# Performance work log

Hardware: AMD Instinct MI355X
Metric: run time of the kernel (lower is better)

The kernel has to match this reference:

```python
import jax, jax.numpy as jnp
import numpy as np

SIGMA_SPATIAL = 1.0
SIGMA_BILATERAL = 0.25
RADIUS = 1
PATCH = 2 * RADIUS + 1  # 3


def _spatial_kernel():
    x, y = np.mgrid[-RADIUS:RADIUS + 1, -RADIUS:RADIUS + 1]
    w1 = np.exp(-(x ** 2 + y ** 2) / (2.0 * SIGMA_SPATIAL ** 2))
    return jnp.asarray(w1.reshape(-1), dtype=jnp.float32)  # [PATCH*PATCH]


def _extract_patches(x):
    # x: [B,H,W,C] -> [B,H,W,PATCH*PATCH,C] via reflect-padded shifted slices
    B, H, W, C = x.shape
    xp = jnp.pad(x, ((0, 0), (RADIUS, RADIUS), (RADIUS, RADIUS), (0, 0)), mode='reflect')
    return jnp.stack(
        [xp[:, dy:dy + H, dx:dx + W, :] for dy in range(PATCH) for dx in range(PATCH)],
        axis=3,
    )


def setup_inputs() -> dict:
    key = jax.random.key(0)
    k1, k2 = jax.random.split(key)
    src = jax.random.uniform(k1, (2, 512, 512, 21), dtype=jnp.float32)
    im = jax.random.uniform(k2, (2, 512, 512, 3), dtype=jnp.float32)
    return {"src": src, "im": im}


def reference(src, im):
    w1 = _spatial_kernel()  # [9]
    im_patches = _extract_patches(im)                      # [B,H,W,9,Ci]
    diff2 = jnp.sum((im_patches - im[:, :, :, None, :]) ** 2, axis=-1)  # [B,H,W,9]
    w = jnp.exp(-diff2 / (2.0 * SIGMA_BILATERAL ** 2)) * w1            # [B,H,W,9]
    src_patches = _extract_patches(src)                    # [B,H,W,9,Cs]
    num = jnp.sum(src_patches * w[..., None], axis=3)      # [B,H,W,Cs]
    den = jnp.sum(w, axis=3, keepdims=True)                # [B,H,W,1]
    return num / den
```

## Files before the change

kernel.cpp:

```cpp
#include <hip/hip_runtime.h>

#define BATCH 2
#define H 512
#define W 512
#define CS 21
#define CI 3
#define P 256
#define TPB 256
#define NCH 6

__device__ __forceinline__ int reflect1(int v, int n) {
    if (v < 0) v = -v;
    else if (v >= n) v = 2 * n - 2 - v;
    return v;
}

__device__ __forceinline__ void fma4(float4& a, const float4 v, const float w) {
    a.x = fmaf(v.x, w, a.x);
    a.y = fmaf(v.y, w, a.y);
    a.z = fmaf(v.z, w, a.z);
    a.w = fmaf(v.w, w, a.w);
}

__global__ __launch_bounds__(TPB) void jbu_kernel(
    const float* __restrict__ src, const float* __restrict__ im,
    float* __restrict__ out)
{
    __shared__ __align__(16) float s_im[3][P + 2][CI];
    __shared__ __align__(16) float s_w[P][12];

    const int t  = threadIdx.x;
    const int x0 = blockIdx.x * P;
    const int y  = blockIdx.y;
    const int b  = blockIdx.z;

    const int ry0 = reflect1(y - 1, H);
    const int ry2 = reflect1(y + 1, H);

    for (int i = t; i < 3 * (P + 2) * CI; i += TPB) {
        int r   = i / ((P + 2) * CI);
        int rem = i - r * ((P + 2) * CI);
        int col = rem / CI;
        int ch  = rem - col * CI;
        int ry  = (r == 0) ? ry0 : ((r == 1) ? y : ry2);
        int gx  = reflect1(x0 + col - 1, W);
        s_im[r][col][ch] = im[((b * H + ry) * W + gx) * CI + ch];
    }
    __syncthreads();

    {
        const float w1k[9] = {0.36787944f, 0.60653066f, 0.36787944f,
                              0.60653066f, 1.0f,        0.60653066f,
                              0.36787944f, 0.60653066f, 0.36787944f};
        const float c0 = s_im[1][t + 1][0];
        const float c1 = s_im[1][t + 1][1];
        const float c2 = s_im[1][t + 1][2];
        float wv[9];
        float den = 0.f;
        #pragma unroll
        for (int k = 0; k < 9; ++k) {
            const int dy = k / 3, dx = k % 3;
            float d0 = s_im[dy][t + dx][0] - c0;
            float d1 = s_im[dy][t + dx][1] - c1;
            float d2 = s_im[dy][t + dx][2] - c2;
            float w = __expf(-8.0f * (d0 * d0 + d1 * d1 + d2 * d2)) * w1k[k];
            wv[k] = w;
            den += w;
        }
        const float inv = 1.0f / den;
        float4 wa = {wv[0] * inv, wv[1] * inv, wv[2] * inv, wv[3] * inv};
        float4 wb = {wv[4] * inv, wv[5] * inv, wv[6] * inv, wv[7] * inv};
        *(float4*)&s_w[t][0] = wa;
        *(float4*)&s_w[t][4] = wb;
        s_w[t][8] = wv[8] * inv;
    }
    __syncthreads();

    const float* row0 = src + (size_t)(b * H + ry0) * (W * CS);
    const float* row1 = src + (size_t)(b * H + y  ) * (W * CS);
    const float* row2 = src + (size_t)(b * H + ry2) * (W * CS);
    float*       orow = out + (size_t)(b * H + y  ) * (W * CS);

    for (int wi = t; wi < P * NCH; wi += TPB) {
        int p = wi / NCH;
        int q = wi - p * NCH;
        int coff = (q == 5) ? 17 : (q << 2);
        int x  = x0 + p;
        int xm = (x == 0)     ? 1     : x - 1;
        int xp = (x == W - 1) ? W - 2 : x + 1;
        int om = xm * CS + coff;
        int oc = x  * CS + coff;
        int op = xp * CS + coff;

        const float4 wA = *(const float4*)&s_w[p][0];
        const float4 wB = *(const float4*)&s_w[p][4];
        const float  w8 = s_w[p][8];

        float4 v0 = *(const float4*)(row0 + om);
        float4 v1 = *(const float4*)(row0 + oc);
        float4 v2 = *(const float4*)(row0 + op);
        float4 v3 = *(const float4*)(row1 + om);
        float4 v4 = *(const float4*)(row1 + oc);
        float4 v5 = *(const float4*)(row1 + op);
        float4 v6 = *(const float4*)(row2 + om);
        float4 v7 = *(const float4*)(row2 + oc);
        float4 v8 = *(const float4*)(row2 + op);

        float4 acc = {0.f, 0.f, 0.f, 0.f};
        fma4(acc, v0, wA.x);
        fma4(acc, v1, wA.y);
        fma4(acc, v2, wA.z);
        fma4(acc, v3, wA.w);
        fma4(acc, v4, wB.x);
        fma4(acc, v5, wB.y);
        fma4(acc, v6, wB.z);
        fma4(acc, v7, wB.w);
        fma4(acc, v8, w8);

        *(float4*)(orow + oc) = acc;
    }
}

extern "C" void kernel_launch(void* const* d_in, const int* in_sizes, int n_in,
                              void* d_out, int out_size, void* d_ws, size_t ws_size,
                              hipStream_t stream) {
    const float* src = (const float*)d_in[0];
    const float* im  = (const float*)d_in[1];
    float* out = (float*)d_out;
    dim3 grid(W / P, H, BATCH);
    jbu_kernel<<<grid, TPB, 0, stream>>>(src, im, out);
}
```

Measured before the change: 114.7 us.

## Remap blocks so each XCD handles contiguous rows and alias shared buffers

```diff
diff --git a/kernel.cpp b/kernel.cpp
--- a/kernel.cpp
+++ b/kernel.cpp
@@ -9,12 +9,6 @@
 #define TPB 256
 #define NCH 6
 
-__device__ __forceinline__ int reflect1(int v, int n) {
-    if (v < 0) v = -v;
-    else if (v >= n) v = 2 * n - 2 - v;
-    return v;
-}
-
 __device__ __forceinline__ void fma4(float4& a, const float4 v, const float w) {
     a.x = fmaf(v.x, w, a.x);
     a.y = fmaf(v.y, w, a.y);
@@ -22,58 +16,71 @@
     a.w = fmaf(v.w, w, a.w);
 }
 
-__global__ __launch_bounds__(TPB) void jbu_kernel(
+__global__ __launch_bounds__(TPB, 8) void jbu_kernel(
     const float* __restrict__ src, const float* __restrict__ im,
     float* __restrict__ out)
 {
-    __shared__ __align__(16) float s_im[3][P + 2][CI];
-    __shared__ __align__(16) float s_w[P][12];
+    __shared__ __align__(16) float s_buf[P * 12];
 
-    const int t  = threadIdx.x;
-    const int x0 = blockIdx.x * P;
-    const int y  = blockIdx.y;
-    const int b  = blockIdx.z;
+    const int t = threadIdx.x;
 
-    const int ry0 = reflect1(y - 1, H);
-    const int ry2 = reflect1(y + 1, H);
+    const int f   = blockIdx.x;
+    const int xcd = f & 7;
+    const int g   = f >> 3;
+    const int y   = (xcd << 6) | (g & 63);
+    const int r   = g >> 6;
+    const int x0  = (r & 1) * P;
+    const int b   = r >> 1;
 
+    const int ry0 = (y == 0)     ? 1     : y - 1;
+    const int ry2 = (y == H - 1) ? H - 2 : y + 1;
+
+    const float* imb = im + (size_t)b * H * W * CI;
     for (int i = t; i < 3 * (P + 2) * CI; i += TPB) {
-        int r   = i / ((P + 2) * CI);
-        int rem = i - r * ((P + 2) * CI);
+        int row = i / ((P + 2) * CI);
+        int rem = i - row * ((P + 2) * CI);
         int col = rem / CI;
         int ch  = rem - col * CI;
-        int ry  = (r == 0) ? ry0 : ((r == 1) ? y : ry2);
-        int gx  = reflect1(x0 + col - 1, W);
-        s_im[r][col][ch] = im[((b * H + ry) * W + gx) * CI + ch];
+        int ry  = (row == 0) ? ry0 : ((row == 1) ? y : ry2);
+        int gx  = x0 + col - 1;
+        gx = (gx < 0) ? 1 : ((gx >= W) ? W - 2 : gx);
+        s_buf[i] = imb[(ry * W + gx) * CI + ch];
     }
     __syncthreads();
 
+    float4 wa, wb;
+    float w8n;
     {
         const float w1k[9] = {0.36787944f, 0.60653066f, 0.36787944f,
                               0.60653066f, 1.0f,        0.60653066f,
                               0.36787944f, 0.60653066f, 0.36787944f};
-        const float c0 = s_im[1][t + 1][0];
-        const float c1 = s_im[1][t + 1][1];
-        const float c2 = s_im[1][t + 1][2];
+        const int cbase = ((P + 2) + t + 1) * CI;
+        const float c0 = s_buf[cbase + 0];
+        const float c1 = s_buf[cbase + 1];
+        const float c2 = s_buf[cbase + 2];
         float wv[9];
         float den = 0.f;
         #pragma unroll
         for (int k = 0; k < 9; ++k) {
             const int dy = k / 3, dx = k % 3;
-            float d0 = s_im[dy][t + dx][0] - c0;
-            float d1 = s_im[dy][t + dx][1] - c1;
-            float d2 = s_im[dy][t + dx][2] - c2;
+            const int idx = (dy * (P + 2) + t + dx) * CI;
+            float d0 = s_buf[idx + 0] - c0;
+            float d1 = s_buf[idx + 1] - c1;
+            float d2 = s_buf[idx + 2] - c2;
             float w = __expf(-8.0f * (d0 * d0 + d1 * d1 + d2 * d2)) * w1k[k];
             wv[k] = w;
             den += w;
         }
         const float inv = 1.0f / den;
-        float4 wa = {wv[0] * inv, wv[1] * inv, wv[2] * inv, wv[3] * inv};
-        float4 wb = {wv[4] * inv, wv[5] * inv, wv[6] * inv, wv[7] * inv};
-        *(float4*)&s_w[t][0] = wa;
-        *(float4*)&s_w[t][4] = wb;
-        s_w[t][8] = wv[8] * inv;
+        wa = make_float4(wv[0] * inv, wv[1] * inv, wv[2] * inv, wv[3] * inv);
+        wb = make_float4(wv[4] * inv, wv[5] * inv, wv[6] * inv, wv[7] * inv);
+        w8n = wv[8] * inv;
     }
+    __syncthreads();
+
+    *(float4*)&s_buf[t * 12 + 0] = wa;
+    *(float4*)&s_buf[t * 12 + 4] = wb;
+    s_buf[t * 12 + 8] = w8n;
     __syncthreads();
 
     const float* row0 = src + (size_t)(b * H + ry0) * (W * CS);
@@ -92,9 +99,9 @@
         int oc = x  * CS + coff;
         int op = xp * CS + coff;
 
-        const float4 wA = *(const float4*)&s_w[p][0];
-        const float4 wB = *(const float4*)&s_w[p][4];
-        const float  w8 = s_w[p][8];
+        const float4 pwA = *(const float4*)&s_buf[p * 12 + 0];
+        const float4 pwB = *(const float4*)&s_buf[p * 12 + 4];
+        const float  pw8 = s_buf[p * 12 + 8];
 
         float4 v0 = *(const float4*)(row0 + om);
         float4 v1 = *(const float4*)(row0 + oc);
@@ -107,15 +114,15 @@
         float4 v8 = *(const float4*)(row2 + op);
 
         float4 acc = {0.f, 0.f, 0.f, 0.f};
-        fma4(acc, v0, wA.x);
-        fma4(acc, v1, wA.y);
-        fma4(acc, v2, wA.z);
-        fma4(acc, v3, wA.w);
-        fma4(acc, v4, wB.x);
-        fma4(acc, v5, wB.y);
-        fma4(acc, v6, wB.z);
-        fma4(acc, v7, wB.w);
-        fma4(acc, v8, w8);
+        fma4(acc, v0, pwA.x);
+        fma4(acc, v1, pwA.y);
+        fma4(acc, v2, pwA.z);
+        fma4(acc, v3, pwA.w);
+        fma4(acc, v4, pwB.x);
+        fma4(acc, v5, pwB.y);
+        fma4(acc, v6, pwB.z);
+        fma4(acc, v7, pwB.w);
+        fma4(acc, v8, pw8);
 
         *(float4*)(orow + oc) = acc;
     }
@@ -127,6 +134,6 @@
     const float* src = (const float*)d_in[0];
     const float* im  = (const float*)d_in[1];
     float* out = (float*)d_out;
-    dim3 grid(W / P, H, BATCH);
+    dim3 grid((W / P) * H * BATCH, 1, 1);
     jbu_kernel<<<grid, TPB, 0, stream>>>(src, im, out);
 }
```

After: 112.6 us. No clear change (-1.8%).
